# Performance work log

Measured on AMD Instinct MI355X. Metric: run time of the kernel, lower is better.

The kernel has to match this reference:

```python
import jax, jax.numpy as jnp
import numpy as np

N_NODES = 50000
N_EDGES = 800000
IN_DIM = 100
OUT_DIM = 40
K_HOPS = 3


def setup_inputs() -> dict:
    key = jax.random.key(0)
    k1, k2, k3, k4 = jax.random.split(key, 4)
    feat = jax.random.normal(k1, (N_NODES, IN_DIM), dtype=jnp.float32)
    # fc params (PyTorch Linear default init scale ~ 1/sqrt(in_dim))
    W = jax.random.normal(k2, (OUT_DIM, IN_DIM), dtype=jnp.float32) / np.sqrt(IN_DIM)
    b = jnp.zeros((OUT_DIM,), dtype=jnp.float32)
    src = jax.random.randint(k3, (N_EDGES,), 0, N_NODES, dtype=jnp.int32)
    dst = jax.random.randint(k4, (N_EDGES,), 0, N_NODES, dtype=jnp.int32)
    return {"feat": feat, "W": W, "b": b, "src": src, "dst": dst}


def reference(feat, W, b, src, dst):
    n = feat.shape[0]
    # symmetric degree norm (DGL SGConv uses in-degrees, clamp(min=1))
    deg = jax.ops.segment_sum(jnp.ones_like(dst, dtype=feat.dtype), dst, num_segments=n)
    norm = jnp.maximum(deg, 1.0)[:, None] ** -0.5  # [N,1]
    h = feat
    for _ in range(K_HOPS):
        h = h * norm
        # SpMM: sum over incoming edges (gather src rows, scatter-add to dst)
        h = jax.ops.segment_sum(h[src], dst, num_segments=n)
        h = h * norm
    # user-supplied normalize: per-feature zero mean / unit std (unbiased std)
    h = (h - h.mean(axis=0)) / h.std(axis=0, ddof=1)
    # final linear classifier
    return h @ W.T + b
```

## Files before the change

kernel.cpp:

```cpp
#include <hip/hip_runtime.h>

#define N_NODES 50000
#define N_EDGES 800000
#define IN_DIM 100
#define OUT_DIM 40
#define ROW 50
#define ROW_PAD 64
#define SCAN_B 512
#define NSCAN_BLK ((N_NODES + SCAN_B - 1) / SCAN_B)
#define CSR_CAP (N_EDGES + N_NODES * 8 + 64)

typedef unsigned int uint;

__device__ __forceinline__ float bflo(uint u) { return __uint_as_float(u << 16); }
__device__ __forceinline__ float bfhi(uint u) { return __uint_as_float(u & 0xffff0000u); }
__device__ __forceinline__ uint packbf(float a, float b) {
    uint ua = __float_as_uint(a), ub = __float_as_uint(b);
    ua = (ua + 0x7fffu + ((ua >> 16) & 1u)) >> 16;
    ub = (ub + 0x7fffu + ((ub >> 16) & 1u)) >> 16;
    return ua | (ub << 16);
}

__global__ void zero_kernel(int* p, int n, uint* fs, uint* bufA, uint* bufB) {
    int i = blockIdx.x * blockDim.x + threadIdx.x;
    if (i < n) p[i] = 0;
    if (i < ROW_PAD) {
        fs[(size_t)N_NODES * ROW_PAD + i] = 0u;
        bufA[(size_t)N_NODES * ROW_PAD + i] = 0u;
        bufB[(size_t)N_NODES * ROW_PAD + i] = 0u;
    }
}

__global__ void deg_kernel(const int* __restrict__ dst, int* __restrict__ deg,
                           int* __restrict__ eoff) {
    int e = blockIdx.x * blockDim.x + threadIdx.x;
    if (e < N_EDGES) eoff[e] = atomicAdd(&deg[dst[e]], 1);
}

__global__ __launch_bounds__(SCAN_B) void scan1_kernel(const int* __restrict__ deg,
                                                       int* __restrict__ rowptr,
                                                       float* __restrict__ norm,
                                                       float* __restrict__ norm2,
                                                       int* __restrict__ blocksum) {
    int i = blockIdx.x * SCAN_B + threadIdx.x;
    int lane = threadIdx.x & 63, wid = threadIdx.x >> 6;
    int d = (i < N_NODES) ? deg[i] : 0;
    int da = (d + 7) & ~7;
    int v = da;
#pragma unroll
    for (int off = 1; off < 64; off <<= 1) {
        int t = __shfl_up(v, off);
        if (lane >= off) v += t;
    }
    __shared__ int wsum[8];
    if (lane == 63) wsum[wid] = v;
    __syncthreads();
    if (threadIdx.x < 8) {
        int w = wsum[threadIdx.x];
#pragma unroll
        for (int off = 1; off < 8; off <<= 1) {
            int t = __shfl_up(w, off);
            if (lane >= off) w += t;
        }
        wsum[threadIdx.x] = w;
    }
    __syncthreads();
    int woff = wid ? wsum[wid - 1] : 0;
    int incl = woff + v;
    if (i < N_NODES) {
        rowptr[i] = incl - da;
        float n1 = 1.0f / sqrtf((float)max(d, 1));
        norm[i] = n1;
        norm2[i] = n1 * n1;
    }
    if (threadIdx.x == SCAN_B - 1) blocksum[blockIdx.x] = incl;
}

__global__ __launch_bounds__(128) void scan2_kernel(const int* __restrict__ blocksum,
                                                    int* __restrict__ blockoff,
                                                    int* __restrict__ rowptr) {
    __shared__ int s[128];
    int t = threadIdx.x;
    int v = (t < NSCAN_BLK) ? blocksum[t] : 0;
    s[t] = v;
    __syncthreads();
    for (int off = 1; off < 128; off <<= 1) {
        int u = (t >= off) ? s[t - off] : 0;
        __syncthreads();
        s[t] += u;
        __syncthreads();
    }
    if (t < NSCAN_BLK) blockoff[t] = s[t] - v;
    if (t == 127) rowptr[N_NODES] = s[127];
}

__global__ __launch_bounds__(SCAN_B) void scan3_kernel(int* __restrict__ rowptr,
                                                       const int* __restrict__ blockoff,
                                                       const int* __restrict__ deg,
                                                       int* __restrict__ csr) {
    int i = blockIdx.x * SCAN_B + threadIdx.x;
    if (i < N_NODES) {
        int rp = rowptr[i] + blockoff[blockIdx.x];
        rowptr[i] = rp;
        int d = deg[i], da = (d + 7) & ~7;
        for (int k = d; k < da; ++k) csr[rp + k] = N_NODES;
    }
}

__global__ void csr_fill_kernel(const int* __restrict__ src, const int* __restrict__ dst,
                                const int* __restrict__ rowptr,
                                const int* __restrict__ eoff,
                                int* __restrict__ csr) {
    int e = blockIdx.x * blockDim.x + threadIdx.x;
    if (e < N_EDGES) csr[rowptr[dst[e]] + eoff[e]] = src[e];
}

__global__ __launch_bounds__(256) void prescale_kernel(const float* __restrict__ feat,
                                                       const float* __restrict__ norm,
                                                       uint4* __restrict__ fs4) {
    int t = blockIdx.x * 256 + threadIdx.x;
    if (t >= N_NODES * 16) return;
    int n = t >> 4, ql = t & 15;
    float nm = norm[n];
    uint4 o = make_uint4(0u, 0u, 0u, 0u);
    const float4* fr = (const float4*)(feat + (size_t)n * IN_DIM);
    if (ql < 12) {
        float4 a = fr[2 * ql], b2 = fr[2 * ql + 1];
        o.x = packbf(a.x * nm, a.y * nm);  o.y = packbf(a.z * nm, a.w * nm);
        o.z = packbf(b2.x * nm, b2.y * nm); o.w = packbf(b2.z * nm, b2.w * nm);
    } else if (ql == 12) {
        float4 a = fr[24];
        o.x = packbf(a.x * nm, a.y * nm);  o.y = packbf(a.z * nm, a.w * nm);
    }
    fs4[t] = o;
}

__global__ __launch_bounds__(128) void spmm_kernel(const uint4* __restrict__ H4,
                                                   const int* __restrict__ rowptr,
                                                   const int* __restrict__ csr,
                                                   const float* __restrict__ scale,
                                                   uint4* __restrict__ out4) {
    const int n = blockIdx.x * 2 + (threadIdx.x >> 6);
    const int l = threadIdx.x & 63;
    const int q = l >> 4;
    const int ql = l & 15;
    const int beg = rowptr[n], end = rowptr[n + 1];
    float ax0 = 0.f, ax1 = 0.f, ax2 = 0.f, ax3 = 0.f;
    float ay0 = 0.f, ay1 = 0.f, ay2 = 0.f, ay3 = 0.f;
    int j = beg;
    for (; j + 16 <= end; j += 16) {
        int s0 = csr[j + q];
        int s1 = csr[j + 4 + q];
        int s2 = csr[j + 8 + q];
        int s3 = csr[j + 12 + q];
        uint4 u0 = H4[(size_t)s0 * 16 + ql];
        uint4 u1 = H4[(size_t)s1 * 16 + ql];
        uint4 u2 = H4[(size_t)s2 * 16 + ql];
        uint4 u3 = H4[(size_t)s3 * 16 + ql];
        ax0 += bflo(u0.x); ay0 += bfhi(u0.x);
        ax1 += bflo(u0.y); ay1 += bfhi(u0.y);
        ax2 += bflo(u0.z); ay2 += bfhi(u0.z);
        ax3 += bflo(u0.w); ay3 += bfhi(u0.w);
        ax0 += bflo(u1.x); ay0 += bfhi(u1.x);
        ax1 += bflo(u1.y); ay1 += bfhi(u1.y);
        ax2 += bflo(u1.z); ay2 += bfhi(u1.z);
        ax3 += bflo(u1.w); ay3 += bfhi(u1.w);
        ax0 += bflo(u2.x); ay0 += bfhi(u2.x);
        ax1 += bflo(u2.y); ay1 += bfhi(u2.y);
        ax2 += bflo(u2.z); ay2 += bfhi(u2.z);
        ax3 += bflo(u2.w); ay3 += bfhi(u2.w);
        ax0 += bflo(u3.x); ay0 += bfhi(u3.x);
        ax1 += bflo(u3.y); ay1 += bfhi(u3.y);
        ax2 += bflo(u3.z); ay2 += bfhi(u3.z);
        ax3 += bflo(u3.w); ay3 += bfhi(u3.w);
    }
    if (j < end) {
        int s0 = csr[j + q];
        int s1 = csr[j + 4 + q];
        uint4 u0 = H4[(size_t)s0 * 16 + ql];
        uint4 u1 = H4[(size_t)s1 * 16 + ql];
        ax0 += bflo(u0.x); ay0 += bfhi(u0.x);
        ax1 += bflo(u0.y); ay1 += bfhi(u0.y);
        ax2 += bflo(u0.z); ay2 += bfhi(u0.z);
        ax3 += bflo(u0.w); ay3 += bfhi(u0.w);
        ax0 += bflo(u1.x); ay0 += bfhi(u1.x);
        ax1 += bflo(u1.y); ay1 += bfhi(u1.y);
        ax2 += bflo(u1.z); ay2 += bfhi(u1.z);
        ax3 += bflo(u1.w); ay3 += bfhi(u1.w);
    }
    ax0 += __shfl_xor(ax0, 16); ax1 += __shfl_xor(ax1, 16);
    ax2 += __shfl_xor(ax2, 16); ax3 += __shfl_xor(ax3, 16);
    ay0 += __shfl_xor(ay0, 16); ay1 += __shfl_xor(ay1, 16);
    ay2 += __shfl_xor(ay2, 16); ay3 += __shfl_xor(ay3, 16);
    ax0 += __shfl_xor(ax0, 32); ax1 += __shfl_xor(ax1, 32);
    ax2 += __shfl_xor(ax2, 32); ax3 += __shfl_xor(ax3, 32);
    ay0 += __shfl_xor(ay0, 32); ay1 += __shfl_xor(ay1, 32);
    ay2 += __shfl_xor(ay2, 32); ay3 += __shfl_xor(ay3, 32);
    if (q == 0) {
        float sc = scale[n];
        uint4 o;
        o.x = packbf(ax0 * sc, ay0 * sc);
        o.y = packbf(ax1 * sc, ay1 * sc);
        o.z = packbf(ax2 * sc, ay2 * sc);
        o.w = packbf(ax3 * sc, ay3 * sc);
        out4[(size_t)n * 16 + ql] = o;
    }
}

#define CS_BLOCKS 625
#define CS_THREADS 256
__global__ __launch_bounds__(CS_THREADS) void col_stats_kernel(const uint* __restrict__ h,
                                                               float* __restrict__ colsum,
                                                               float* __restrict__ colsq) {
    int gtid = blockIdx.x * CS_THREADS + threadIdx.x;
    const int stride = CS_BLOCKS * CS_THREADS;
    const int total = N_NODES * ROW_PAD;
    float s0 = 0.f, s1 = 0.f, q0 = 0.f, q1 = 0.f;
    for (int i = gtid; i < total; i += stride) {
        uint u = h[i];
        float a = bflo(u), b = bfhi(u);
        s0 += a; s1 += b; q0 += a * a; q1 += b * b;
    }
    __shared__ float ssum[IN_DIM], ssq[IN_DIM];
    if (threadIdx.x < IN_DIM) { ssum[threadIdx.x] = 0.f; ssq[threadIdx.x] = 0.f; }
    __syncthreads();
    int p = gtid & 63;
    if (p < ROW) {
        atomicAdd(&ssum[2 * p], s0);
        atomicAdd(&ssum[2 * p + 1], s1);
        atomicAdd(&ssq[2 * p], q0);
        atomicAdd(&ssq[2 * p + 1], q1);
    }
    __syncthreads();
    if (threadIdx.x < IN_DIM) {
        atomicAdd(&colsum[threadIdx.x], ssum[threadIdx.x]);
        atomicAdd(&colsq[threadIdx.x], ssq[threadIdx.x]);
    }
}

__global__ __launch_bounds__(256) void prep_kernel(const float* __restrict__ colsum,
                                                   const float* __restrict__ colsq,
                                                   const float* __restrict__ W,
                                                   const float* __restrict__ b,
                                                   float* __restrict__ Wt,
                                                   float* __restrict__ bp) {
    __shared__ float smean[IN_DIM];
    __shared__ float sinv[IN_DIM];
    int t = threadIdx.x;
    const float Nf = (float)N_NODES;
    if (t < IN_DIM) {
        float m = colsum[t] / Nf;
        float var = (colsq[t] - Nf * m * m) / (Nf - 1.0f);
        var = fmaxf(var, 1e-20f);
        smean[t] = m;
        sinv[t] = 1.0f / sqrtf(var);
    }
    __syncthreads();
    for (int i = t; i < IN_DIM * OUT_DIM; i += 256) {
        int o = i % OUT_DIM, f = i / OUT_DIM;
        Wt[f * OUT_DIM + o] = W[o * IN_DIM + f] * sinv[f];
    }
    if (t < OUT_DIM) {
        float acc = b[t];
        for (int f = 0; f < IN_DIM; ++f)
            acc -= smean[f] * W[t * IN_DIM + f] * sinv[f];
        bp[t] = acc;
    }
}

__global__ __launch_bounds__(256) void final_kernel(const uint4* __restrict__ h4,
                                                    const float* __restrict__ Wt,
                                                    const float* __restrict__ bp,
                                                    float* __restrict__ out) {
    __shared__ float sW[104 * OUT_DIM];
    __shared__ float sb[OUT_DIM];
    for (int i = threadIdx.x; i < 104 * OUT_DIM; i += 256)
        sW[i] = (i < IN_DIM * OUT_DIM) ? Wt[i] : 0.f;
    if (threadIdx.x < OUT_DIM) sb[threadIdx.x] = bp[threadIdx.x];
    __syncthreads();
    int t = blockIdx.x * 256 + threadIdx.x;
    if (t >= N_NODES * 10) return;
    int n = t / 10;
    int og = (t - n * 10) * 4;
    const uint4* hr = h4 + (size_t)n * 16;
    float a0 = sb[og], a1 = sb[og + 1], a2 = sb[og + 2], a3 = sb[og + 3];
#pragma unroll
    for (int r = 0; r < 13; ++r) {
        uint4 u = hr[r];
        int f = r * 8;
        float v0 = bflo(u.x), v1 = bfhi(u.x), v2 = bflo(u.y), v3 = bfhi(u.y);
        float v4 = bflo(u.z), v5 = bfhi(u.z), v6 = bflo(u.w), v7 = bfhi(u.w);
        const float* w0 = &sW[(f + 0) * OUT_DIM + og];
        const float* w1 = &sW[(f + 1) * OUT_DIM + og];
        const float* w2 = &sW[(f + 2) * OUT_DIM + og];
        const float* w3 = &sW[(f + 3) * OUT_DIM + og];
        const float* w4 = &sW[(f + 4) * OUT_DIM + og];
        const float* w5 = &sW[(f + 5) * OUT_DIM + og];
        const float* w6 = &sW[(f + 6) * OUT_DIM + og];
        const float* w7 = &sW[(f + 7) * OUT_DIM + og];
        a0 += v0 * w0[0] + v1 * w1[0] + v2 * w2[0] + v3 * w3[0]
            + v4 * w4[0] + v5 * w5[0] + v6 * w6[0] + v7 * w7[0];
        a1 += v0 * w0[1] + v1 * w1[1] + v2 * w2[1] + v3 * w3[1]
            + v4 * w4[1] + v5 * w5[1] + v6 * w6[1] + v7 * w7[1];
        a2 += v0 * w0[2] + v1 * w1[2] + v2 * w2[2] + v3 * w3[2]
            + v4 * w4[2] + v5 * w5[2] + v6 * w6[2] + v7 * w7[2];
        a3 += v0 * w0[3] + v1 * w1[3] + v2 * w2[3] + v3 * w3[3]
            + v4 * w4[3] + v5 * w5[3] + v6 * w6[3] + v7 * w7[3];
    }
    float4 o = make_float4(a0, a1, a2, a3);
    *((float4*)(out + (size_t)n * OUT_DIM + og)) = o;
}

extern "C" void kernel_launch(void* const* d_in, const int* in_sizes, int n_in,
                              void* d_out, int out_size, void* d_ws, size_t ws_size,
                              hipStream_t stream) {
    const float* feat = (const float*)d_in[0];
    const float* W    = (const float*)d_in[1];
    const float* b    = (const float*)d_in[2];
    const int*   src  = (const int*)d_in[3];
    const int*   dst  = (const int*)d_in[4];
    float* out = (float*)d_out;

    char* w = (char*)d_ws;
    int*   deg      = (int*)w;    w += N_NODES * 4;
    float* colsum   = (float*)w;  w += 128 * 4;
    float* colsq    = (float*)w;  w += 128 * 4;
    int*   eoff     = (int*)w;    w += N_EDGES * 4;
    int*   rowptr   = (int*)w;    w += 50004 * 4;
    float* norm     = (float*)w;  w += N_NODES * 4;
    float* norm2    = (float*)w;  w += N_NODES * 4;
    int*   blocksum = (int*)w;    w += 128 * 4;
    int*   blockoff = (int*)w;    w += 128 * 4;
    int*   csr      = (int*)w;    w += CSR_CAP * 4;
    float* Wt       = (float*)w;  w += IN_DIM * OUT_DIM * 4;
    float* bp       = (float*)w;  w += 64 * 4;
    w = (char*)(((size_t)w + 255) & ~(size_t)255);
    const size_t HB = (size_t)(N_NODES + 1) * ROW_PAD * 4;
    uint*  fs       = (uint*)w;   w += HB;
    uint*  bufA     = (uint*)w;   w += HB;
    uint*  bufB     = (uint*)w;   w += HB;

    {
        int nz = N_NODES + 256;
        zero_kernel<<<(nz + 255) / 256, 256, 0, stream>>>(deg, nz, fs, bufA, bufB);
    }
    deg_kernel<<<(N_EDGES + 255) / 256, 256, 0, stream>>>(dst, deg, eoff);
    scan1_kernel<<<NSCAN_BLK, SCAN_B, 0, stream>>>(deg, rowptr, norm, norm2, blocksum);
    scan2_kernel<<<1, 128, 0, stream>>>(blocksum, blockoff, rowptr);
    scan3_kernel<<<NSCAN_BLK, SCAN_B, 0, stream>>>(rowptr, blockoff, deg, csr);
    csr_fill_kernel<<<(N_EDGES + 255) / 256, 256, 0, stream>>>(src, dst, rowptr, eoff, csr);
    prescale_kernel<<<(N_NODES * 16 + 255) / 256, 256, 0, stream>>>(feat, norm, (uint4*)fs);
    spmm_kernel<<<N_NODES / 2, 128, 0, stream>>>((const uint4*)fs, rowptr, csr, norm2, (uint4*)bufA);
    spmm_kernel<<<N_NODES / 2, 128, 0, stream>>>((const uint4*)bufA, rowptr, csr, norm2, (uint4*)bufB);
    spmm_kernel<<<N_NODES / 2, 128, 0, stream>>>((const uint4*)bufB, rowptr, csr, norm, (uint4*)bufA);
    col_stats_kernel<<<CS_BLOCKS, CS_THREADS, 0, stream>>>(bufA, colsum, colsq);
    prep_kernel<<<1, 256, 0, stream>>>(colsum, colsq, W, b, Wt, bp);
    {
        int total = N_NODES * 10;
        final_kernel<<<(total + 255) / 256, 256, 0, stream>>>((const uint4*)bufA, Wt, bp, out);
    }
}
```

Baseline: 261.9 us.

## Fuse prescale, three SpMM hops and column stats into one cooperative kernel

Replaces five separate launches (prescale, three SpMM passes, column statistics) with a single persistent cooperative kernel that uses grid-wide syncs between phases. Each wave now loops over nodes in a grid-stride fashion instead of one launch-time block per pair of nodes. This removes launch overhead and inter-kernel gaps, but adds grid.sync costs and fixes the grid size from occupancy (assumes 256 CUs), which may reduce latency hiding in the gather-heavy SpMM phases.

```diff
diff --git a/kernel.cpp b/kernel.cpp
--- a/kernel.cpp
+++ b/kernel.cpp
@@ -1,4 +1,7 @@
 #include <hip/hip_runtime.h>
+#include <hip/hip_cooperative_groups.h>
+
+namespace cg = cooperative_groups;
 
 #define N_NODES 50000
 #define N_EDGES 800000
@@ -115,126 +118,145 @@
     if (e < N_EDGES) csr[rowptr[dst[e]] + eoff[e]] = src[e];
 }
 
-__global__ __launch_bounds__(256) void prescale_kernel(const float* __restrict__ feat,
-                                                       const float* __restrict__ norm,
-                                                       uint4* __restrict__ fs4) {
-    int t = blockIdx.x * 256 + threadIdx.x;
-    if (t >= N_NODES * 16) return;
-    int n = t >> 4, ql = t & 15;
-    float nm = norm[n];
-    uint4 o = make_uint4(0u, 0u, 0u, 0u);
-    const float4* fr = (const float4*)(feat + (size_t)n * IN_DIM);
-    if (ql < 12) {
-        float4 a = fr[2 * ql], b2 = fr[2 * ql + 1];
-        o.x = packbf(a.x * nm, a.y * nm);  o.y = packbf(a.z * nm, a.w * nm);
-        o.z = packbf(b2.x * nm, b2.y * nm); o.w = packbf(b2.z * nm, b2.w * nm);
-    } else if (ql == 12) {
-        float4 a = fr[24];
-        o.x = packbf(a.x * nm, a.y * nm);  o.y = packbf(a.z * nm, a.w * nm);
-    }
-    fs4[t] = o;
-}
-
-__global__ __launch_bounds__(128) void spmm_kernel(const uint4* __restrict__ H4,
-                                                   const int* __restrict__ rowptr,
-                                                   const int* __restrict__ csr,
-                                                   const float* __restrict__ scale,
-                                                   uint4* __restrict__ out4) {
-    const int n = blockIdx.x * 2 + (threadIdx.x >> 6);
+
+__device__ __forceinline__ void spmm_phase(const uint4* __restrict__ H4,
+                                           const int* __restrict__ rowptr,
+                                           const int* __restrict__ csr,
+                                           const float* __restrict__ scale,
+                                           uint4* __restrict__ out4,
+                                           int waveId, int nWaves) {
     const int l = threadIdx.x & 63;
     const int q = l >> 4;
     const int ql = l & 15;
-    const int beg = rowptr[n], end = rowptr[n + 1];
-    float ax0 = 0.f, ax1 = 0.f, ax2 = 0.f, ax3 = 0.f;
-    float ay0 = 0.f, ay1 = 0.f, ay2 = 0.f, ay3 = 0.f;
-    int j = beg;
-    for (; j + 16 <= end; j += 16) {
-        int s0 = csr[j + q];
-        int s1 = csr[j + 4 + q];
-        int s2 = csr[j + 8 + q];
-        int s3 = csr[j + 12 + q];
-        uint4 u0 = H4[(size_t)s0 * 16 + ql];
-        uint4 u1 = H4[(size_t)s1 * 16 + ql];
-        uint4 u2 = H4[(size_t)s2 * 16 + ql];
-        uint4 u3 = H4[(size_t)s3 * 16 + ql];
-        ax0 += bflo(u0.x); ay0 += bfhi(u0.x);
-        ax1 += bflo(u0.y); ay1 += bfhi(u0.y);
-        ax2 += bflo(u0.z); ay2 += bfhi(u0.z);
-        ax3 += bflo(u0.w); ay3 += bfhi(u0.w);
-        ax0 += bflo(u1.x); ay0 += bfhi(u1.x);
-        ax1 += bflo(u1.y); ay1 += bfhi(u1.y);
-        ax2 += bflo(u1.z); ay2 += bfhi(u1.z);
-        ax3 += bflo(u1.w); ay3 += bfhi(u1.w);
-        ax0 += bflo(u2.x); ay0 += bfhi(u2.x);
-        ax1 += bflo(u2.y); ay1 += bfhi(u2.y);
-        ax2 += bflo(u2.z); ay2 += bfhi(u2.z);
-        ax3 += bflo(u2.w); ay3 += bfhi(u2.w);
-        ax0 += bflo(u3.x); ay0 += bfhi(u3.x);
-        ax1 += bflo(u3.y); ay1 += bfhi(u3.y);
-        ax2 += bflo(u3.z); ay2 += bfhi(u3.z);
-        ax3 += bflo(u3.w); ay3 += bfhi(u3.w);
-    }
-    if (j < end) {
-        int s0 = csr[j + q];
-        int s1 = csr[j + 4 + q];
-        uint4 u0 = H4[(size_t)s0 * 16 + ql];
-        uint4 u1 = H4[(size_t)s1 * 16 + ql];
-        ax0 += bflo(u0.x); ay0 += bfhi(u0.x);
-        ax1 += bflo(u0.y); ay1 += bfhi(u0.y);
-        ax2 += bflo(u0.z); ay2 += bfhi(u0.z);
-        ax3 += bflo(u0.w); ay3 += bfhi(u0.w);
-        ax0 += bflo(u1.x); ay0 += bfhi(u1.x);
-        ax1 += bflo(u1.y); ay1 += bfhi(u1.y);
-        ax2 += bflo(u1.z); ay2 += bfhi(u1.z);
-        ax3 += bflo(u1.w); ay3 += bfhi(u1.w);
-    }
-    ax0 += __shfl_xor(ax0, 16); ax1 += __shfl_xor(ax1, 16);
-    ax2 += __shfl_xor(ax2, 16); ax3 += __shfl_xor(ax3, 16);
-    ay0 += __shfl_xor(ay0, 16); ay1 += __shfl_xor(ay1, 16);
-    ay2 += __shfl_xor(ay2, 16); ay3 += __shfl_xor(ay3, 16);
-    ax0 += __shfl_xor(ax0, 32); ax1 += __shfl_xor(ax1, 32);
-    ax2 += __shfl_xor(ax2, 32); ax3 += __shfl_xor(ax3, 32);
-    ay0 += __shfl_xor(ay0, 32); ay1 += __shfl_xor(ay1, 32);
-    ay2 += __shfl_xor(ay2, 32); ay3 += __shfl_xor(ay3, 32);
-    if (q == 0) {
-        float sc = scale[n];
-        uint4 o;
-        o.x = packbf(ax0 * sc, ay0 * sc);
-        o.y = packbf(ax1 * sc, ay1 * sc);
-        o.z = packbf(ax2 * sc, ay2 * sc);
-        o.w = packbf(ax3 * sc, ay3 * sc);
-        out4[(size_t)n * 16 + ql] = o;
-    }
-}
-
-#define CS_BLOCKS 625
-#define CS_THREADS 256
-__global__ __launch_bounds__(CS_THREADS) void col_stats_kernel(const uint* __restrict__ h,
-                                                               float* __restrict__ colsum,
-                                                               float* __restrict__ colsq) {
-    int gtid = blockIdx.x * CS_THREADS + threadIdx.x;
-    const int stride = CS_BLOCKS * CS_THREADS;
-    const int total = N_NODES * ROW_PAD;
-    float s0 = 0.f, s1 = 0.f, q0 = 0.f, q1 = 0.f;
-    for (int i = gtid; i < total; i += stride) {
-        uint u = h[i];
-        float a = bflo(u), b = bfhi(u);
-        s0 += a; s1 += b; q0 += a * a; q1 += b * b;
-    }
-    __shared__ float ssum[IN_DIM], ssq[IN_DIM];
-    if (threadIdx.x < IN_DIM) { ssum[threadIdx.x] = 0.f; ssq[threadIdx.x] = 0.f; }
-    __syncthreads();
-    int p = gtid & 63;
-    if (p < ROW) {
-        atomicAdd(&ssum[2 * p], s0);
-        atomicAdd(&ssum[2 * p + 1], s1);
-        atomicAdd(&ssq[2 * p], q0);
-        atomicAdd(&ssq[2 * p + 1], q1);
-    }
-    __syncthreads();
-    if (threadIdx.x < IN_DIM) {
-        atomicAdd(&colsum[threadIdx.x], ssum[threadIdx.x]);
-        atomicAdd(&colsq[threadIdx.x], ssq[threadIdx.x]);
+    for (int n = waveId; n < N_NODES; n += nWaves) {
+        const int beg = rowptr[n], end = rowptr[n + 1];
+        float ax0 = 0.f, ax1 = 0.f, ax2 = 0.f, ax3 = 0.f;
+        float ay0 = 0.f, ay1 = 0.f, ay2 = 0.f, ay3 = 0.f;
+        int j = beg;
+        for (; j + 16 <= end; j += 16) {
+            int s0 = csr[j + q];
+            int s1 = csr[j + 4 + q];
+            int s2 = csr[j + 8 + q];
+            int s3 = csr[j + 12 + q];
+            uint4 u0 = H4[(size_t)s0 * 16 + ql];
+            uint4 u1 = H4[(size_t)s1 * 16 + ql];
+            uint4 u2 = H4[(size_t)s2 * 16 + ql];
+            uint4 u3 = H4[(size_t)s3 * 16 + ql];
+            ax0 += bflo(u0.x); ay0 += bfhi(u0.x);
+            ax1 += bflo(u0.y); ay1 += bfhi(u0.y);
+            ax2 += bflo(u0.z); ay2 += bfhi(u0.z);
+            ax3 += bflo(u0.w); ay3 += bfhi(u0.w);
+            ax0 += bflo(u1.x); ay0 += bfhi(u1.x);
+            ax1 += bflo(u1.y); ay1 += bfhi(u1.y);
+            ax2 += bflo(u1.z); ay2 += bfhi(u1.z);
+            ax3 += bflo(u1.w); ay3 += bfhi(u1.w);
+            ax0 += bflo(u2.x); ay0 += bfhi(u2.x);
+            ax1 += bflo(u2.y); ay1 += bfhi(u2.y);
+            ax2 += bflo(u2.z); ay2 += bfhi(u2.z);
+            ax3 += bflo(u2.w); ay3 += bfhi(u2.w);
+            ax0 += bflo(u3.x); ay0 += bfhi(u3.x);
+            ax1 += bflo(u3.y); ay1 += bfhi(u3.y);
+            ax2 += bflo(u3.z); ay2 += bfhi(u3.z);
+            ax3 += bflo(u3.w); ay3 += bfhi(u3.w);
+        }
+        if (j < end) {
+            int s0 = csr[j + q];
+            int s1 = csr[j + 4 + q];
+            uint4 u0 = H4[(size_t)s0 * 16 + ql];
+            uint4 u1 = H4[(size_t)s1 * 16 + ql];
+            ax0 += bflo(u0.x); ay0 += bfhi(u0.x);
+            ax1 += bflo(u0.y); ay1 += bfhi(u0.y);
+            ax2 += bflo(u0.z); ay2 += bfhi(u0.z);
+            ax3 += bflo(u0.w); ay3 += bfhi(u0.w);
+            ax0 += bflo(u1.x); ay0 += bfhi(u1.x);
+            ax1 += bflo(u1.y); ay1 += bfhi(u1.y);
+            ax2 += bflo(u1.z); ay2 += bfhi(u1.z);
+            ax3 += bflo(u1.w); ay3 += bfhi(u1.w);
+        }
+        ax0 += __shfl_xor(ax0, 16); ax1 += __shfl_xor(ax1, 16);
+        ax2 += __shfl_xor(ax2, 16); ax3 += __shfl_xor(ax3, 16);
+        ay0 += __shfl_xor(ay0, 16); ay1 += __shfl_xor(ay1, 16);
+        ay2 += __shfl_xor(ay2, 16); ay3 += __shfl_xor(ay3, 16);
+        ax0 += __shfl_xor(ax0, 32); ax1 += __shfl_xor(ax1, 32);
+        ax2 += __shfl_xor(ax2, 32); ax3 += __shfl_xor(ax3, 32);
+        ay0 += __shfl_xor(ay0, 32); ay1 += __shfl_xor(ay1, 32);
+        ay2 += __shfl_xor(ay2, 32); ay3 += __shfl_xor(ay3, 32);
+        if (q == 0) {
+            float sc = scale[n];
+            uint4 o;
+            o.x = packbf(ax0 * sc, ay0 * sc);
+            o.y = packbf(ax1 * sc, ay1 * sc);
+            o.z = packbf(ax2 * sc, ay2 * sc);
+            o.w = packbf(ax3 * sc, ay3 * sc);
+            out4[(size_t)n * 16 + ql] = o;
+        }
+    }
+}
+
+__global__ __launch_bounds__(256) void fused_mid_kernel(const float* __restrict__ feat,
+                                                        const float* __restrict__ norm,
+                                                        const float* __restrict__ norm2,
+                                                        const int* __restrict__ rowptr,
+                                                        const int* __restrict__ csr,
+                                                        uint4* __restrict__ fs4,
+                                                        uint4* __restrict__ bufA4,
+                                                        uint4* __restrict__ bufB4,
+                                                        float* __restrict__ colsum,
+                                                        float* __restrict__ colsq) {
+    cg::grid_group grid = cg::this_grid();
+    const int gt = blockIdx.x * 256 + threadIdx.x;
+    const int gsz = gridDim.x * 256;
+
+    for (int t = gt; t < N_NODES * 16; t += gsz) {
+        int n = t >> 4, ql = t & 15;
+        float nm = norm[n];
+        uint4 o = make_uint4(0u, 0u, 0u, 0u);
+        const float4* fr = (const float4*)(feat + (size_t)n * IN_DIM);
+        if (ql < 12) {
+            float4 a = fr[2 * ql], b2 = fr[2 * ql + 1];
+            o.x = packbf(a.x * nm, a.y * nm);  o.y = packbf(a.z * nm, a.w * nm);
+            o.z = packbf(b2.x * nm, b2.y * nm); o.w = packbf(b2.z * nm, b2.w * nm);
+        } else if (ql == 12) {
+            float4 a = fr[24];
+            o.x = packbf(a.x * nm, a.y * nm);  o.y = packbf(a.z * nm, a.w * nm);
+        }
+        fs4[t] = o;
+    }
+    grid.sync();
+
+    const int waveId = blockIdx.x * 4 + (threadIdx.x >> 6);
+    const int nWaves = gridDim.x * 4;
+    spmm_phase(fs4,   rowptr, csr, norm2, bufA4, waveId, nWaves);
+    grid.sync();
+    spmm_phase(bufA4, rowptr, csr, norm2, bufB4, waveId, nWaves);
+    grid.sync();
+    spmm_phase(bufB4, rowptr, csr, norm,  bufA4, waveId, nWaves);
+    grid.sync();
+
+    {
+        const uint* h = (const uint*)bufA4;
+        const int total = N_NODES * ROW_PAD;
+        float s0 = 0.f, s1 = 0.f, q0 = 0.f, q1 = 0.f;
+        for (int i = gt; i < total; i += gsz) {
+            uint u = h[i];
+            float a = bflo(u), b = bfhi(u);
+            s0 += a; s1 += b; q0 += a * a; q1 += b * b;
+        }
+        __shared__ float ssum[IN_DIM], ssq[IN_DIM];
+        if (threadIdx.x < IN_DIM) { ssum[threadIdx.x] = 0.f; ssq[threadIdx.x] = 0.f; }
+        __syncthreads();
+        int p = gt & 63;
+        if (p < ROW) {
+            atomicAdd(&ssum[2 * p], s0);
+            atomicAdd(&ssum[2 * p + 1], s1);
+            atomicAdd(&ssq[2 * p], q0);
+            atomicAdd(&ssq[2 * p + 1], q1);
+        }
+        __syncthreads();
+        if (threadIdx.x < IN_DIM) {
+            atomicAdd(&colsum[threadIdx.x], ssum[threadIdx.x]);
+            atomicAdd(&colsq[threadIdx.x], ssq[threadIdx.x]);
+        }
     }
 }
 
@@ -349,11 +371,25 @@
     scan2_kernel<<<1, 128, 0, stream>>>(blocksum, blockoff, rowptr);
     scan3_kernel<<<NSCAN_BLK, SCAN_B, 0, stream>>>(rowptr, blockoff, deg, csr);
     csr_fill_kernel<<<(N_EDGES + 255) / 256, 256, 0, stream>>>(src, dst, rowptr, eoff, csr);
-    prescale_kernel<<<(N_NODES * 16 + 255) / 256, 256, 0, stream>>>(feat, norm, (uint4*)fs);
-    spmm_kernel<<<N_NODES / 2, 128, 0, stream>>>((const uint4*)fs, rowptr, csr, norm2, (uint4*)bufA);
-    spmm_kernel<<<N_NODES / 2, 128, 0, stream>>>((const uint4*)bufA, rowptr, csr, norm2, (uint4*)bufB);
-    spmm_kernel<<<N_NODES / 2, 128, 0, stream>>>((const uint4*)bufB, rowptr, csr, norm, (uint4*)bufA);
-    col_stats_kernel<<<CS_BLOCKS, CS_THREADS, 0, stream>>>(bufA, colsum, colsq);
+    {
+        static int maxBlkPerCU = 0;
+        if (maxBlkPerCU == 0) {
+            hipOccupancyMaxActiveBlocksPerMultiprocessor(&maxBlkPerCU,
+                (const void*)fused_mid_kernel, 256, 0);
+            if (maxBlkPerCU <= 0) maxBlkPerCU = 2;
+        }
+        int grid = maxBlkPerCU * 256;
+        if (grid > 2048) grid = 2048;
+        uint4* fs4   = (uint4*)fs;
+        uint4* bufA4 = (uint4*)bufA;
+        uint4* bufB4 = (uint4*)bufB;
+        void* args[] = { (void*)&feat, (void*)&norm, (void*)&norm2,
+                         (void*)&rowptr, (void*)&csr,
+                         (void*)&fs4, (void*)&bufA4, (void*)&bufB4,
+                         (void*)&colsum, (void*)&colsq };
+        hipLaunchCooperativeKernel((const void*)fused_mid_kernel,
+                                   dim3(grid), dim3(256), args, 0, stream);
+    }
     prep_kernel<<<1, 256, 0, stream>>>(colsum, colsq, W, b, Wt, bp);
     {
         int total = N_NODES * 10;
```

After: 729.8 us. 2.79x slower.

## Fuse scan2 into scan3, merge CSR fill with prescale, fold prep into final

Applied to the files above, without the earlier changes.

Removes three kernel launches. The single-block scan2 is dropped: each scan3 block now sums the preceding block totals itself with a wavefront reduction. CSR fill and feature prescale become one launch split by block index. The weight-normalization prep is recomputed redundantly in every final_kernel block. The aim is to cut launch gaps and serialization, at the cost of redundant per-block work in scan3 and final_kernel.

```diff
diff --git a/kernel.cpp b/kernel.cpp
--- a/kernel.cpp
+++ b/kernel.cpp
@@ -9,6 +9,8 @@
 #define SCAN_B 512
 #define NSCAN_BLK ((N_NODES + SCAN_B - 1) / SCAN_B)
 #define CSR_CAP (N_EDGES + N_NODES * 8 + 64)
+#define CSRF_BLOCKS ((N_EDGES + 255) / 256)
+#define PRE_BLOCKS ((N_NODES * 16 + 255) / 256)
 
 typedef unsigned int uint;
 
@@ -76,63 +78,61 @@
     if (threadIdx.x == SCAN_B - 1) blocksum[blockIdx.x] = incl;
 }
 
-__global__ __launch_bounds__(128) void scan2_kernel(const int* __restrict__ blocksum,
-                                                    int* __restrict__ blockoff,
-                                                    int* __restrict__ rowptr) {
-    __shared__ int s[128];
-    int t = threadIdx.x;
-    int v = (t < NSCAN_BLK) ? blocksum[t] : 0;
-    s[t] = v;
-    __syncthreads();
-    for (int off = 1; off < 128; off <<= 1) {
-        int u = (t >= off) ? s[t - off] : 0;
-        __syncthreads();
-        s[t] += u;
-        __syncthreads();
-    }
-    if (t < NSCAN_BLK) blockoff[t] = s[t] - v;
-    if (t == 127) rowptr[N_NODES] = s[127];
-}
-
 __global__ __launch_bounds__(SCAN_B) void scan3_kernel(int* __restrict__ rowptr,
-                                                       const int* __restrict__ blockoff,
+                                                       const int* __restrict__ blocksum,
                                                        const int* __restrict__ deg,
                                                        int* __restrict__ csr) {
-    int i = blockIdx.x * SCAN_B + threadIdx.x;
+    __shared__ int s_off;
+    const int b = blockIdx.x;
+    if (threadIdx.x < 64) {
+        int lane = threadIdx.x;
+        int v = (lane < b) ? blocksum[lane] : 0;
+        if (lane + 64 < b) v += blocksum[lane + 64];
+#pragma unroll
+        for (int off = 32; off >= 1; off >>= 1) v += __shfl_xor(v, off);
+        if (lane == 0) s_off = v;
+    }
+    __syncthreads();
+    const int boff = s_off;
+    int i = b * SCAN_B + threadIdx.x;
     if (i < N_NODES) {
-        int rp = rowptr[i] + blockoff[blockIdx.x];
+        int rp = rowptr[i] + boff;
         rowptr[i] = rp;
         int d = deg[i], da = (d + 7) & ~7;
         for (int k = d; k < da; ++k) csr[rp + k] = N_NODES;
     }
-}
-
-__global__ void csr_fill_kernel(const int* __restrict__ src, const int* __restrict__ dst,
-                                const int* __restrict__ rowptr,
-                                const int* __restrict__ eoff,
-                                int* __restrict__ csr) {
-    int e = blockIdx.x * blockDim.x + threadIdx.x;
-    if (e < N_EDGES) csr[rowptr[dst[e]] + eoff[e]] = src[e];
-}
-
-__global__ __launch_bounds__(256) void prescale_kernel(const float* __restrict__ feat,
-                                                       const float* __restrict__ norm,
-                                                       uint4* __restrict__ fs4) {
-    int t = blockIdx.x * 256 + threadIdx.x;
-    if (t >= N_NODES * 16) return;
-    int n = t >> 4, ql = t & 15;
-    float nm = norm[n];
-    uint4 o = make_uint4(0u, 0u, 0u, 0u);
-    const float4* fr = (const float4*)(feat + (size_t)n * IN_DIM);
-    if (ql < 12) {
-        float4 a = fr[2 * ql], b2 = fr[2 * ql + 1];
-        o.x = packbf(a.x * nm, a.y * nm);  o.y = packbf(a.z * nm, a.w * nm);
-        o.z = packbf(b2.x * nm, b2.y * nm); o.w = packbf(b2.z * nm, b2.w * nm);
-    } else if (ql == 12) {
-        float4 a = fr[24];
-        o.x = packbf(a.x * nm, a.y * nm);  o.y = packbf(a.z * nm, a.w * nm);
-    }
-    fs4[t] = o;
+    if (b == NSCAN_BLK - 1 && threadIdx.x == 0)
+        rowptr[N_NODES] = boff + blocksum[b];
+}
+
+__global__ __launch_bounds__(256) void fill_prescale_kernel(const int* __restrict__ src,
+                                                            const int* __restrict__ dst,
+                                                            const int* __restrict__ rowptr,
+                                                            const int* __restrict__ eoff,
+                                                            int* __restrict__ csr,
+                                                            const float* __restrict__ feat,
+                                                            const float* __restrict__ norm,
+                                                            uint4* __restrict__ fs4) {
+    if (blockIdx.x < CSRF_BLOCKS) {
+        int e = blockIdx.x * 256 + threadIdx.x;
+        if (e < N_EDGES) csr[rowptr[dst[e]] + eoff[e]] = src[e];
+    } else {
+        int t = (blockIdx.x - CSRF_BLOCKS) * 256 + threadIdx.x;
+        if (t >= N_NODES * 16) return;
+        int n = t >> 4, ql = t & 15;
+        float nm = norm[n];
+        uint4 o = make_uint4(0u, 0u, 0u, 0u);
+        const float4* fr = (const float4*)(feat + (size_t)n * IN_DIM);
+        if (ql < 12) {
+            float4 a = fr[2 * ql], b2 = fr[2 * ql + 1];
+            o.x = packbf(a.x * nm, a.y * nm);  o.y = packbf(a.z * nm, a.w * nm);
+            o.z = packbf(b2.x * nm, b2.y * nm); o.w = packbf(b2.z * nm, b2.w * nm);
+        } else if (ql == 12) {
+            float4 a = fr[24];
+            o.x = packbf(a.x * nm, a.y * nm);  o.y = packbf(a.z * nm, a.w * nm);
+        }
+        fs4[t] = o;
+    }
 }
 
 __global__ __launch_bounds__(128) void spmm_kernel(const uint4* __restrict__ H4,
@@ -238,47 +238,39 @@
     }
 }
 
-__global__ __launch_bounds__(256) void prep_kernel(const float* __restrict__ colsum,
-                                                   const float* __restrict__ colsq,
-                                                   const float* __restrict__ W,
-                                                   const float* __restrict__ b,
-                                                   float* __restrict__ Wt,
-                                                   float* __restrict__ bp) {
-    __shared__ float smean[IN_DIM];
-    __shared__ float sinv[IN_DIM];
-    int t = threadIdx.x;
-    const float Nf = (float)N_NODES;
-    if (t < IN_DIM) {
-        float m = colsum[t] / Nf;
-        float var = (colsq[t] - Nf * m * m) / (Nf - 1.0f);
-        var = fmaxf(var, 1e-20f);
-        smean[t] = m;
-        sinv[t] = 1.0f / sqrtf(var);
-    }
-    __syncthreads();
-    for (int i = t; i < IN_DIM * OUT_DIM; i += 256) {
-        int o = i % OUT_DIM, f = i / OUT_DIM;
-        Wt[f * OUT_DIM + o] = W[o * IN_DIM + f] * sinv[f];
-    }
-    if (t < OUT_DIM) {
-        float acc = b[t];
-        for (int f = 0; f < IN_DIM; ++f)
-            acc -= smean[f] * W[t * IN_DIM + f] * sinv[f];
-        bp[t] = acc;
-    }
-}
-
 __global__ __launch_bounds__(256) void final_kernel(const uint4* __restrict__ h4,
-                                                    const float* __restrict__ Wt,
-                                                    const float* __restrict__ bp,
+                                                    const float* __restrict__ colsum,
+                                                    const float* __restrict__ colsq,
+                                                    const float* __restrict__ W,
+                                                    const float* __restrict__ bvec,
                                                     float* __restrict__ out) {
     __shared__ float sW[104 * OUT_DIM];
     __shared__ float sb[OUT_DIM];
-    for (int i = threadIdx.x; i < 104 * OUT_DIM; i += 256)
-        sW[i] = (i < IN_DIM * OUT_DIM) ? Wt[i] : 0.f;
-    if (threadIdx.x < OUT_DIM) sb[threadIdx.x] = bp[threadIdx.x];
-    __syncthreads();
-    int t = blockIdx.x * 256 + threadIdx.x;
+    __shared__ float smean[IN_DIM];
+    __shared__ float sinv[IN_DIM];
+    const int tid = threadIdx.x;
+    const float Nf = (float)N_NODES;
+    if (tid < IN_DIM) {
+        float m = colsum[tid] / Nf;
+        float var = (colsq[tid] - Nf * m * m) / (Nf - 1.0f);
+        var = fmaxf(var, 1e-20f);
+        smean[tid] = m;
+        sinv[tid] = 1.0f / sqrtf(var);
+    }
+    __syncthreads();
+    for (int i = tid; i < 104 * OUT_DIM; i += 256) {
+        int f = i / OUT_DIM, o = i % OUT_DIM;
+        sW[i] = (f < IN_DIM) ? W[o * IN_DIM + f] * sinv[f] : 0.f;
+    }
+    __syncthreads();
+    if (tid < OUT_DIM) {
+        float acc = bvec[tid];
+        for (int f = 0; f < IN_DIM; ++f)
+            acc -= smean[f] * sW[f * OUT_DIM + tid];
+        sb[tid] = acc;
+    }
+    __syncthreads();
+    int t = blockIdx.x * 256 + tid;
     if (t >= N_NODES * 10) return;
     int n = t / 10;
     int og = (t - n * 10) * 4;
@@ -330,10 +322,7 @@
     float* norm     = (float*)w;  w += N_NODES * 4;
     float* norm2    = (float*)w;  w += N_NODES * 4;
     int*   blocksum = (int*)w;    w += 128 * 4;
-    int*   blockoff = (int*)w;    w += 128 * 4;
     int*   csr      = (int*)w;    w += CSR_CAP * 4;
-    float* Wt       = (float*)w;  w += IN_DIM * OUT_DIM * 4;
-    float* bp       = (float*)w;  w += 64 * 4;
     w = (char*)(((size_t)w + 255) & ~(size_t)255);
     const size_t HB = (size_t)(N_NODES + 1) * ROW_PAD * 4;
     uint*  fs       = (uint*)w;   w += HB;
@@ -346,17 +335,16 @@
     }
     deg_kernel<<<(N_EDGES + 255) / 256, 256, 0, stream>>>(dst, deg, eoff);
     scan1_kernel<<<NSCAN_BLK, SCAN_B, 0, stream>>>(deg, rowptr, norm, norm2, blocksum);
-    scan2_kernel<<<1, 128, 0, stream>>>(blocksum, blockoff, rowptr);
-    scan3_kernel<<<NSCAN_BLK, SCAN_B, 0, stream>>>(rowptr, blockoff, deg, csr);
-    csr_fill_kernel<<<(N_EDGES + 255) / 256, 256, 0, stream>>>(src, dst, rowptr, eoff, csr);
-    prescale_kernel<<<(N_NODES * 16 + 255) / 256, 256, 0, stream>>>(feat, norm, (uint4*)fs);
+    scan3_kernel<<<NSCAN_BLK, SCAN_B, 0, stream>>>(rowptr, blocksum, deg, csr);
+    fill_prescale_kernel<<<CSRF_BLOCKS + PRE_BLOCKS, 256, 0, stream>>>(
+        src, dst, rowptr, eoff, csr, feat, norm, (uint4*)fs);
     spmm_kernel<<<N_NODES / 2, 128, 0, stream>>>((const uint4*)fs, rowptr, csr, norm2, (uint4*)bufA);
     spmm_kernel<<<N_NODES / 2, 128, 0, stream>>>((const uint4*)bufA, rowptr, csr, norm2, (uint4*)bufB);
     spmm_kernel<<<N_NODES / 2, 128, 0, stream>>>((const uint4*)bufB, rowptr, csr, norm, (uint4*)bufA);
     col_stats_kernel<<<CS_BLOCKS, CS_THREADS, 0, stream>>>(bufA, colsum, colsq);
-    prep_kernel<<<1, 256, 0, stream>>>(colsum, colsq, W, b, Wt, bp);
     {
         int total = N_NODES * 10;
-        final_kernel<<<(total + 255) / 256, 256, 0, stream>>>((const uint4*)bufA, Wt, bp, out);
-    }
-}
+        final_kernel<<<(total + 255) / 256, 256, 0, stream>>>(
+            (const uint4*)bufA, colsum, colsq, W, b, out);
+    }
+}
```

Measured after the change: 258.3 us. No clear change (-1.4%).
